# Performance work log

Measured on AMD Instinct MI355X. Metric: run time of the kernel, lower is better.

## Reference

```python
import jax, jax.numpy as jnp
import numpy as np

B, S, D = 4, 2048, 1024

def setup_inputs() -> dict:
    key = jax.random.key(0)
    ks = jax.random.split(key, 7)
    s = 1.0 / np.sqrt(D)
    return {
        "x":  jax.random.normal(ks[0], (B, S, D), dtype=jnp.float32),
        "Wq": jax.random.uniform(ks[1], (D, D), jnp.float32, -s, s),
        "bq": jax.random.uniform(ks[2], (D,),  jnp.float32, -s, s),
        "Wk": jax.random.uniform(ks[3], (D, D), jnp.float32, -s, s),
        "bk": jax.random.uniform(ks[4], (D,),  jnp.float32, -s, s),
        "Wv": jax.random.uniform(ks[5], (D, D), jnp.float32, -s, s),
        "bv": jax.random.uniform(ks[6], (D,),  jnp.float32, -s, s),
    }

def reference(x, Wq, bq, Wk, bk, Wv, bv):
    # Q/K/V projections: [B,S,D]
    Q = jnp.einsum('bsd,de->bse', x, Wq) + bq
    K = jnp.einsum('bsd,de->bse', x, Wk) + bk
    V = jnp.einsum('bsd,de->bse', x, Wv) + bv
    scale = 1.0 / jnp.sqrt(jnp.asarray(K.shape[-1], K.dtype))
    scores = jnp.einsum('bqd,bkd->bqk', Q, K) * scale  # [B,S,S]
    weights = jax.nn.softmax(scores, axis=-1)
    return jnp.einsum('bqk,bkd->bqd', weights, V)
```

## Files before the change

kernel.cpp:

```cpp
#include <hip/hip_runtime.h>

typedef __attribute__((ext_vector_type(4))) float f32x4;
typedef __attribute__((ext_vector_type(8))) short bf16x8;

__device__ __forceinline__ float bf2f(unsigned short u) {
  union { unsigned int i; float f; } x; x.i = ((unsigned int)u) << 16; return x.f;
}
__device__ __forceinline__ unsigned short f2bf(float f) {
  union { float f; unsigned int i; } x; x.f = f;
  unsigned int r = (x.i + 0x7FFFu + ((x.i >> 16) & 1u)) >> 16;
  return (unsigned short)r;
}

#define BARX __builtin_amdgcn_s_barrier()
#define LGK0 asm volatile("s_waitcnt lgkmcnt(0)" ::: "memory")
#define VM0  asm volatile("s_waitcnt vmcnt(0)" ::: "memory")
#define GLD(gsrc, ldsoff)                                                        \
  __builtin_amdgcn_global_load_lds(                                              \
      (const __attribute__((address_space(1))) void*)(gsrc),                     \
      (__attribute__((address_space(3))) void*)&lds[ldsoff], 16, 0, 0)

__global__ __launch_bounds__(256) void cvt_f2b(const float* __restrict__ src,
                                               unsigned short* __restrict__ dst, long n4) {
  long i = (long)blockIdx.x * 256 + threadIdx.x;
  long stride = (long)gridDim.x * 256;
  for (; i < n4; i += stride) {
    float4 v = *(const float4*)&src[i * 4];
    ushort4 o;
    o.x = f2bf(v.x); o.y = f2bf(v.y); o.z = f2bf(v.z); o.w = f2bf(v.w);
    *(ushort4*)&dst[i * 4] = o;
  }
}

__global__ __launch_bounds__(256) void transpose_f2b(const float* __restrict__ src,
                                                     unsigned short* __restrict__ dst,
                                                     int rows, int cols) {
  __shared__ float t[32][33];
  int bx = blockIdx.x * 32, by = blockIdx.y * 32;
  int tx = threadIdx.x, ty = threadIdx.y;
#pragma unroll
  for (int k = 0; k < 4; ++k)
    t[ty + 8 * k][tx] = src[(long)(by + ty + 8 * k) * cols + bx + tx];
  __syncthreads();
#pragma unroll
  for (int k = 0; k < 4; ++k)
    dst[(long)(bx + ty + 8 * k) * rows + by + tx] = f2bf(t[tx][ty + 8 * k]);
}

__global__ __launch_bounds__(512) void transpose_v(const unsigned short* __restrict__ src,
                                                   unsigned short* __restrict__ dst) {
  __shared__ unsigned short t[64][65];
  const long sb = (long)blockIdx.z * 2048 * 3072;
  const long db = (long)blockIdx.z * 1024 * 2064;
  const int d0 = blockIdx.x * 64;
  const int s0 = blockIdx.y * 64;
  const int tx = threadIdx.x, ty = threadIdx.y;
#pragma unroll
  for (int k = 0; k < 8; ++k)
    t[ty + 8 * k][tx] = src[sb + (long)(s0 + ty + 8 * k) * 3072 + d0 + tx];
  __syncthreads();
#pragma unroll
  for (int k = 0; k < 8; ++k)
    dst[db + (long)(d0 + ty + 8 * k) * 2064 + s0 + tx] = t[tx][ty + 8 * k];
}

template <int MODE>
__global__ __launch_bounds__(256, 2) void gemms(const unsigned short* __restrict__ Ap_,
                                                const unsigned short* __restrict__ Bp_,
                                                void* __restrict__ Cv,
                                                const float* __restrict__ q_,
                                                const float* __restrict__ k_,
                                                const float* __restrict__ v_,
                                                int Kd, int lda, int ldb, int ldc, float scale,
                                                long sA, long sB, long sC) {
  __shared__ unsigned short lds[32768];
  int bx, by, bz;
  if (MODE == 2) {
    const int flat = blockIdx.x;
    const int nid = ((flat & 7) << 6) | (flat >> 3);
    bx = nid & 15; by = (nid >> 4) & 7; bz = nid >> 7;
  } else {
    bx = blockIdx.x; by = blockIdx.y; bz = blockIdx.z;
  }
  const unsigned short* Ap = Ap_ + (long)bz * sA;
  const unsigned short* Bp = Bp_ + (long)bz * sB;
  const int tid = threadIdx.x;
  const int m0 = bx * 128, n0 = by * 128;
  const int lane = tid & 63, wave = tid >> 6;
  const int wm = wave >> 1, wn = wave & 1;
  const int rr = tid >> 3;
  const int cSrc = ((tid & 7) ^ (rr & 7)) << 3;
  const int lc = lane & 15, lr = lane >> 4;
  const int x0 = (lc & 4) << 3;
  const int x1 = 32 ^ x0;
  const int klo = (lr << 3) ^ ((lc & 3) << 3);
  const int aoff = (wm * 64 + lc) * 64 + klo;
  const int boff = 8192 + (wn * 64 + lc) * 64 + klo;
  const int NT = Kd >> 6;
  const int rS = tid >> 1;
  const int g0 = (tid & 1) * 4;

  const unsigned short* pA = Ap + (long)(m0 + rr) * lda + cSrc;
  const unsigned short* pB = Bp + (long)(n0 + rr) * ldb + cSrc;
  const long a32 = (long)32 * lda, b32 = (long)32 * ldb;
#define STA(so)                                                                   \
  { GLD(pA, (so) + tid * 8);            GLD(pA + a32, (so) + 2048 + tid * 8);     \
    GLD(pA + 2 * a32, (so) + 4096 + tid * 8); GLD(pA + 3 * a32, (so) + 6144 + tid * 8); }
#define STB(so)                                                                   \
  { GLD(pB, (so) + 8192 + tid * 8);     GLD(pB + b32, (so) + 10240 + tid * 8);    \
    GLD(pB + 2 * b32, (so) + 12288 + tid * 8); GLD(pB + 3 * b32, (so) + 14336 + tid * 8); }

  f32x4 acc[4][4] = {};
  float esum = 0.0f;

  STA(0); STB(0);
  pA += 64; pB += 64;
  VM0;
  BARX;

  for (int t = 0; t < NT; ++t) {
    const int p = t & 1;
    const int soq = (p ^ 1) << 14;
    const unsigned short* Lp = &lds[p << 14];
    const bool pf = (t + 1 < NT);
    bf16x8 a0[2][2], a1[2][2], bb[4][2];
#pragma unroll
    for (int ni = 0; ni < 4; ++ni) {
      bb[ni][0] = *(const bf16x8*)&Lp[boff + ni * 1024 + x0];
      bb[ni][1] = *(const bf16x8*)&Lp[boff + ni * 1024 + x1];
    }
#pragma unroll
    for (int mi = 0; mi < 2; ++mi) {
      a0[mi][0] = *(const bf16x8*)&Lp[aoff + mi * 1024 + x0];
      a0[mi][1] = *(const bf16x8*)&Lp[aoff + mi * 1024 + x1];
    }
    if (pf) STA(soq);
    BARX; LGK0;
    __builtin_amdgcn_s_setprio(1);
#pragma unroll
    for (int mi = 0; mi < 2; ++mi)
#pragma unroll
      for (int ni = 0; ni < 4; ++ni)
#pragma unroll
        for (int x = 0; x < 2; ++x)
          acc[mi][ni] = __builtin_amdgcn_mfma_f32_16x16x32_bf16(
              a0[mi][x], bb[ni][x], acc[mi][ni], 0, 0, 0);
    __builtin_amdgcn_s_setprio(0);
    BARX;
#pragma unroll
    for (int mi = 0; mi < 2; ++mi) {
      a1[mi][0] = *(const bf16x8*)&Lp[aoff + 2048 + mi * 1024 + x0];
      a1[mi][1] = *(const bf16x8*)&Lp[aoff + 2048 + mi * 1024 + x1];
    }
    if (MODE == 2) {
#pragma unroll
      for (int j = 0; j < 4; ++j) {
        bf16x8 s = *(const bf16x8*)&Lp[rS * 64 + (((g0 + j) ^ (rS & 7)) << 3)];
#pragma unroll
        for (int e = 0; e < 8; ++e) esum += bf2f((unsigned short)s[e]);
      }
    }
    if (pf) STB(soq);
    BARX; LGK0;
    __builtin_amdgcn_s_setprio(1);
#pragma unroll
    for (int mi = 0; mi < 2; ++mi)
#pragma unroll
      for (int ni = 0; ni < 4; ++ni)
#pragma unroll
        for (int x = 0; x < 2; ++x)
          acc[2 + mi][ni] = __builtin_amdgcn_mfma_f32_16x16x32_bf16(
              a1[mi][x], bb[ni][x], acc[2 + mi][ni], 0, 0, 0);
    __builtin_amdgcn_s_setprio(0);
    VM0;
    BARX;
    pA += 64; pB += 64;
  }
#undef STA
#undef STB

  const int r0 = m0 + wm * 64 + lr * 4;
  const int c0 = n0 + wn * 64 + lc;
  if (MODE == 2) {
    esum += __shfl_xor(esum, 1);
    float* sums = (float*)lds;
    if ((tid & 1) == 0) sums[tid >> 1] = esum;
    __syncthreads();
    float* O = (float*)Cv + (long)bz * sC;
#pragma unroll
    for (int mi = 0; mi < 4; ++mi)
#pragma unroll
      for (int r = 0; r < 4; ++r) {
        const int l = wm * 64 + mi * 16 + lr * 4 + r;
        const float iv = 1.0f / sums[l];
#pragma unroll
        for (int ni = 0; ni < 4; ++ni)
          O[(long)(m0 + l) * ldc + (c0 + ni * 16)] = acc[mi][ni][r] * iv;
      }
  } else {
    unsigned short* C = (unsigned short*)Cv + (long)bz * sC;
#pragma unroll
    for (int ni = 0; ni < 4; ++ni) {
      const int col = c0 + ni * 16;
      float bv = 0.0f;
      if (MODE == 0)
        bv = (col < 1024) ? q_[col] : ((col < 2048) ? k_[col - 1024] : v_[col - 2048]);
#pragma unroll
      for (int mi = 0; mi < 4; ++mi)
#pragma unroll
        for (int r = 0; r < 4; ++r) {
          float val = acc[mi][ni][r];
          val = (MODE == 0) ? (val + bv) : __expf(val * scale);
          C[(long)(r0 + mi * 16 + r) * ldc + col] = f2bf(val);
        }
    }
  }
}

extern "C" void kernel_launch(void* const* d_in, const int* in_sizes, int n_in,
                              void* d_out, int out_size, void* d_ws, size_t ws_size,
                              hipStream_t stream) {
  const float* x  = (const float*)d_in[0];
  const float* Wq = (const float*)d_in[1];
  const float* bq = (const float*)d_in[2];
  const float* Wk = (const float*)d_in[3];
  const float* bk = (const float*)d_in[4];
  const float* Wv = (const float*)d_in[5];
  const float* bv = (const float*)d_in[6];
  float* out = (float*)d_out;

  const int Bb = 4, S = 2048, D = 1024;
  const long MS = (long)Bb * S;
  const int LDP = 2064;

  char* ws = (char*)d_ws;
  unsigned short* xb  = (unsigned short*)(ws);
  unsigned short* Wt  = (unsigned short*)(ws + (16L << 20));
  unsigned short* QKV = (unsigned short*)(ws + (22L << 20));
  unsigned short* Sc  = (unsigned short*)(ws + (70L << 20));
  unsigned short* VT  = xb;

  cvt_f2b<<<2048, 256, 0, stream>>>(x, xb, MS * D / 4);

  dim3 tb(32, 8);
  dim3 tg(D / 32, D / 32);
  transpose_f2b<<<tg, tb, 0, stream>>>(Wq, Wt, D, D);
  transpose_f2b<<<tg, tb, 0, stream>>>(Wk, Wt + 1024 * 1024, D, D);
  transpose_f2b<<<tg, tb, 0, stream>>>(Wv, Wt + 2 * 1024 * 1024, D, D);

  dim3 pgrid(MS / 128, 3072 / 128, 1);
  gemms<0><<<pgrid, 256, 0, stream>>>(xb, Wt, QKV, bq, bk, bv,
                                      D, D, D, 3072, 1.0f, 0, 0, 0);

  dim3 vtb(64, 8);
  dim3 vtg(D / 64, S / 64, Bb);
  transpose_v<<<vtg, vtb, 0, stream>>>(QKV + 2048, VT);

  dim3 sgrid(S / 128, S / 128, Bb);
  gemms<1><<<sgrid, 256, 0, stream>>>(QKV, QKV + 1024, Sc, nullptr, nullptr, nullptr,
                                      D, 3072, 3072, LDP, 1.0f / 32.0f,
                                      (long)S * 3072, (long)S * 3072, (long)S * LDP);

  gemms<2><<<512, 256, 0, stream>>>(Sc, VT, out, nullptr, nullptr, nullptr,
                                    2048, LDP, LDP, D, 1.0f,
                                    (long)S * LDP, (long)D * LDP, (long)S * D);
}
```

Before: 173.2 us.

## Restructure GEMM main loop into 4-stage BK=32 pipeline with MFMA row sums

After: 195.0 us. 12.6% more time.

```diff
diff --git a/kernel.cpp b/kernel.cpp
--- a/kernel.cpp
+++ b/kernel.cpp
@@ -14,7 +14,6 @@
 
 #define BARX __builtin_amdgcn_s_barrier()
 #define LGK0 asm volatile("s_waitcnt lgkmcnt(0)" ::: "memory")
-#define VM0  asm volatile("s_waitcnt vmcnt(0)" ::: "memory")
 #define GLD(gsrc, ldsoff)                                                        \
   __builtin_amdgcn_global_load_lds(                                              \
       (const __attribute__((address_space(1))) void*)(gsrc),                     \
@@ -65,7 +64,7 @@
 }
 
 template <int MODE>
-__global__ __launch_bounds__(256, 2) void gemms(const unsigned short* __restrict__ Ap_,
+__global__ __launch_bounds__(256, 2) void gemmk(const unsigned short* __restrict__ Ap_,
                                                 const unsigned short* __restrict__ Bp_,
                                                 void* __restrict__ Cv,
                                                 const float* __restrict__ q_,
@@ -82,120 +81,80 @@
   } else {
     bx = blockIdx.x; by = blockIdx.y; bz = blockIdx.z;
   }
-  const unsigned short* Ap = Ap_ + (long)bz * sA;
-  const unsigned short* Bp = Bp_ + (long)bz * sB;
   const int tid = threadIdx.x;
   const int m0 = bx * 128, n0 = by * 128;
   const int lane = tid & 63, wave = tid >> 6;
   const int wm = wave >> 1, wn = wave & 1;
-  const int rr = tid >> 3;
-  const int cSrc = ((tid & 7) ^ (rr & 7)) << 3;
+  const int rrS = tid >> 2;
+  const int gS = (((tid & 3) ^ ((tid >> 2) & 3)) << 3);
   const int lc = lane & 15, lr = lane >> 4;
-  const int x0 = (lc & 4) << 3;
-  const int x1 = 32 ^ x0;
-  const int klo = (lr << 3) ^ ((lc & 3) << 3);
-  const int aoff = (wm * 64 + lc) * 64 + klo;
-  const int boff = 8192 + (wn * 64 + lc) * 64 + klo;
-  const int NT = Kd >> 6;
-  const int rS = tid >> 1;
-  const int g0 = (tid & 1) * 4;
-
-  const unsigned short* pA = Ap + (long)(m0 + rr) * lda + cSrc;
-  const unsigned short* pB = Bp + (long)(n0 + rr) * ldb + cSrc;
-  const long a32 = (long)32 * lda, b32 = (long)32 * ldb;
-#define STA(so)                                                                   \
-  { GLD(pA, (so) + tid * 8);            GLD(pA + a32, (so) + 2048 + tid * 8);     \
-    GLD(pA + 2 * a32, (so) + 4096 + tid * 8); GLD(pA + 3 * a32, (so) + 6144 + tid * 8); }
-#define STB(so)                                                                   \
-  { GLD(pB, (so) + 8192 + tid * 8);     GLD(pB + b32, (so) + 10240 + tid * 8);    \
-    GLD(pB + 2 * b32, (so) + 12288 + tid * 8); GLD(pB + 3 * b32, (so) + 14336 + tid * 8); }
+  const int kof = ((lr ^ (lc & 3)) << 3);
+  const int aoff = (wm * 64 + lc) * 32 + kof;
+  const int boff = 4096 + (wn * 64 + lc) * 32 + kof;
+  const int NT = Kd >> 5;
+
+  const unsigned short* pA0 = Ap_ + (long)bz * sA + (long)(m0 + rrS) * lda + gS;
+  const unsigned short* pA1 = pA0 + (long)64 * lda;
+  const unsigned short* pB0 = Bp_ + (long)bz * sB + (long)(n0 + rrS) * ldb + gS;
+  const unsigned short* pB1 = pB0 + (long)64 * ldb;
+#define STAGE(so)                                                                 \
+  { GLD(pA0, (so) + tid * 8);        GLD(pA1, (so) + 2048 + tid * 8);             \
+    GLD(pB0, (so) + 4096 + tid * 8); GLD(pB1, (so) + 6144 + tid * 8); }
+#define ADV { pA0 += 32; pA1 += 32; pB0 += 32; pB1 += 32; }
 
   f32x4 acc[4][4] = {};
-  float esum = 0.0f;
-
-  STA(0); STB(0);
-  pA += 64; pB += 64;
-  VM0;
+  f32x4 es[4] = {};
+  bf16x8 ones;
+#pragma unroll
+  for (int j = 0; j < 8; ++j) ones[j] = (short)0x3F80;
+
+  STAGE(0); ADV;
+  STAGE(8192); ADV;
+  asm volatile("s_waitcnt vmcnt(4)" ::: "memory");
   BARX;
 
   for (int t = 0; t < NT; ++t) {
-    const int p = t & 1;
-    const int soq = (p ^ 1) << 14;
-    const unsigned short* Lp = &lds[p << 14];
-    const bool pf = (t + 1 < NT);
-    bf16x8 a0[2][2], a1[2][2], bb[4][2];
-#pragma unroll
-    for (int ni = 0; ni < 4; ++ni) {
-      bb[ni][0] = *(const bf16x8*)&Lp[boff + ni * 1024 + x0];
-      bb[ni][1] = *(const bf16x8*)&Lp[boff + ni * 1024 + x1];
+    const int Lb = (t & 3) << 13;
+    const bool pf = (t + 2 < NT);
+    bf16x8 a[4], b[4];
+#pragma unroll
+    for (int mi = 0; mi < 4; ++mi) a[mi] = *(const bf16x8*)&lds[Lb + aoff + mi * 512];
+#pragma unroll
+    for (int ni = 0; ni < 4; ++ni) b[ni] = *(const bf16x8*)&lds[Lb + boff + ni * 512];
+    if (pf) { const int so = ((t + 2) & 3) << 13; STAGE(so); }
+    LGK0;
+    __builtin_amdgcn_s_setprio(1);
+#pragma unroll
+    for (int mi = 0; mi < 4; ++mi)
+#pragma unroll
+      for (int ni = 0; ni < 4; ++ni)
+        acc[mi][ni] = __builtin_amdgcn_mfma_f32_16x16x32_bf16(a[mi], b[ni], acc[mi][ni], 0, 0, 0);
+    if (MODE == 2) {
+#pragma unroll
+      for (int mi = 0; mi < 4; ++mi)
+        es[mi] = __builtin_amdgcn_mfma_f32_16x16x32_bf16(a[mi], ones, es[mi], 0, 0, 0);
     }
-#pragma unroll
-    for (int mi = 0; mi < 2; ++mi) {
-      a0[mi][0] = *(const bf16x8*)&Lp[aoff + mi * 1024 + x0];
-      a0[mi][1] = *(const bf16x8*)&Lp[aoff + mi * 1024 + x1];
-    }
-    if (pf) STA(soq);
-    BARX; LGK0;
-    __builtin_amdgcn_s_setprio(1);
-#pragma unroll
-    for (int mi = 0; mi < 2; ++mi)
-#pragma unroll
-      for (int ni = 0; ni < 4; ++ni)
-#pragma unroll
-        for (int x = 0; x < 2; ++x)
-          acc[mi][ni] = __builtin_amdgcn_mfma_f32_16x16x32_bf16(
-              a0[mi][x], bb[ni][x], acc[mi][ni], 0, 0, 0);
     __builtin_amdgcn_s_setprio(0);
+    if (pf) { asm volatile("s_waitcnt vmcnt(4)" ::: "memory"); }
+    else    { asm volatile("s_waitcnt vmcnt(0)" ::: "memory"); }
     BARX;
-#pragma unroll
-    for (int mi = 0; mi < 2; ++mi) {
-      a1[mi][0] = *(const bf16x8*)&Lp[aoff + 2048 + mi * 1024 + x0];
-      a1[mi][1] = *(const bf16x8*)&Lp[aoff + 2048 + mi * 1024 + x1];
-    }
-    if (MODE == 2) {
-#pragma unroll
-      for (int j = 0; j < 4; ++j) {
-        bf16x8 s = *(const bf16x8*)&Lp[rS * 64 + (((g0 + j) ^ (rS & 7)) << 3)];
-#pragma unroll
-        for (int e = 0; e < 8; ++e) esum += bf2f((unsigned short)s[e]);
-      }
-    }
-    if (pf) STB(soq);
-    BARX; LGK0;
-    __builtin_amdgcn_s_setprio(1);
-#pragma unroll
-    for (int mi = 0; mi < 2; ++mi)
-#pragma unroll
-      for (int ni = 0; ni < 4; ++ni)
-#pragma unroll
-        for (int x = 0; x < 2; ++x)
-          acc[2 + mi][ni] = __builtin_amdgcn_mfma_f32_16x16x32_bf16(
-              a1[mi][x], bb[ni][x], acc[2 + mi][ni], 0, 0, 0);
-    __builtin_amdgcn_s_setprio(0);
-    VM0;
-    BARX;
-    pA += 64; pB += 64;
-  }
-#undef STA
-#undef STB
+    ADV;
+  }
+#undef STAGE
+#undef ADV
 
   const int r0 = m0 + wm * 64 + lr * 4;
   const int c0 = n0 + wn * 64 + lc;
   if (MODE == 2) {
-    esum += __shfl_xor(esum, 1);
-    float* sums = (float*)lds;
-    if ((tid & 1) == 0) sums[tid >> 1] = esum;
-    __syncthreads();
     float* O = (float*)Cv + (long)bz * sC;
 #pragma unroll
     for (int mi = 0; mi < 4; ++mi)
 #pragma unroll
       for (int r = 0; r < 4; ++r) {
-        const int l = wm * 64 + mi * 16 + lr * 4 + r;
-        const float iv = 1.0f / sums[l];
+        const float iv = 1.0f / es[mi][r];
 #pragma unroll
         for (int ni = 0; ni < 4; ++ni)
-          O[(long)(m0 + l) * ldc + (c0 + ni * 16)] = acc[mi][ni][r] * iv;
+          O[(long)(r0 + mi * 16 + r) * ldc + (c0 + ni * 16)] = acc[mi][ni][r] * iv;
       }
   } else {
     unsigned short* C = (unsigned short*)Cv + (long)bz * sC;
@@ -249,7 +208,7 @@
   transpose_f2b<<<tg, tb, 0, stream>>>(Wv, Wt + 2 * 1024 * 1024, D, D);
 
   dim3 pgrid(MS / 128, 3072 / 128, 1);
-  gemms<0><<<pgrid, 256, 0, stream>>>(xb, Wt, QKV, bq, bk, bv,
+  gemmk<0><<<pgrid, 256, 0, stream>>>(xb, Wt, QKV, bq, bk, bv,
                                       D, D, D, 3072, 1.0f, 0, 0, 0);
 
   dim3 vtb(64, 8);
@@ -257,11 +216,11 @@
   transpose_v<<<vtg, vtb, 0, stream>>>(QKV + 2048, VT);
 
   dim3 sgrid(S / 128, S / 128, Bb);
-  gemms<1><<<sgrid, 256, 0, stream>>>(QKV, QKV + 1024, Sc, nullptr, nullptr, nullptr,
+  gemmk<1><<<sgrid, 256, 0, stream>>>(QKV, QKV + 1024, Sc, nullptr, nullptr, nullptr,
                                       D, 3072, 3072, LDP, 1.0f / 32.0f,
                                       (long)S * 3072, (long)S * 3072, (long)S * LDP);
 
-  gemms<2><<<512, 256, 0, stream>>>(Sc, VT, out, nullptr, nullptr, nullptr,
+  gemmk<2><<<512, 256, 0, stream>>>(Sc, VT, out, nullptr, nullptr, nullptr,
                                     2048, LDP, LDP, D, 1.0f,
                                     (long)S * LDP, (long)D * LDP, (long)S * D);
 }
```

## Single-buffer GEMM LDS for higher occupancy and compute row sums via MFMA

Applied to the files above, without the earlier changes.

After: 423.9 us. 145% more time.

```diff
diff --git a/kernel.cpp b/kernel.cpp
--- a/kernel.cpp
+++ b/kernel.cpp
@@ -13,7 +13,6 @@
 }
 
 #define BARX __builtin_amdgcn_s_barrier()
-#define LGK0 asm volatile("s_waitcnt lgkmcnt(0)" ::: "memory")
 #define VM0  asm volatile("s_waitcnt vmcnt(0)" ::: "memory")
 #define GLD(gsrc, ldsoff)                                                        \
   __builtin_amdgcn_global_load_lds(                                              \
@@ -65,7 +64,7 @@
 }
 
 template <int MODE>
-__global__ __launch_bounds__(256, 2) void gemms(const unsigned short* __restrict__ Ap_,
+__global__ __launch_bounds__(256, 4) void gemmo(const unsigned short* __restrict__ Ap_,
                                                 const unsigned short* __restrict__ Bp_,
                                                 void* __restrict__ Cv,
                                                 const float* __restrict__ q_,
@@ -73,7 +72,7 @@
                                                 const float* __restrict__ v_,
                                                 int Kd, int lda, int ldb, int ldc, float scale,
                                                 long sA, long sB, long sC) {
-  __shared__ unsigned short lds[32768];
+  __shared__ unsigned short lds[16384];
   int bx, by, bz;
   if (MODE == 2) {
     const int flat = blockIdx.x;
@@ -82,8 +81,6 @@
   } else {
     bx = blockIdx.x; by = blockIdx.y; bz = blockIdx.z;
   }
-  const unsigned short* Ap = Ap_ + (long)bz * sA;
-  const unsigned short* Bp = Bp_ + (long)bz * sB;
   const int tid = threadIdx.x;
   const int m0 = bx * 128, n0 = by * 128;
   const int lane = tid & 63, wave = tid >> 6;
@@ -97,45 +94,35 @@
   const int aoff = (wm * 64 + lc) * 64 + klo;
   const int boff = 8192 + (wn * 64 + lc) * 64 + klo;
   const int NT = Kd >> 6;
-  const int rS = tid >> 1;
-  const int g0 = (tid & 1) * 4;
-
-  const unsigned short* pA = Ap + (long)(m0 + rr) * lda + cSrc;
-  const unsigned short* pB = Bp + (long)(n0 + rr) * ldb + cSrc;
+
+  const unsigned short* pA = Ap_ + (long)bz * sA + (long)(m0 + rr) * lda + cSrc;
+  const unsigned short* pB = Bp_ + (long)bz * sB + (long)(n0 + rr) * ldb + cSrc;
   const long a32 = (long)32 * lda, b32 = (long)32 * ldb;
-#define STA(so)                                                                   \
-  { GLD(pA, (so) + tid * 8);            GLD(pA + a32, (so) + 2048 + tid * 8);     \
-    GLD(pA + 2 * a32, (so) + 4096 + tid * 8); GLD(pA + 3 * a32, (so) + 6144 + tid * 8); }
-#define STB(so)                                                                   \
-  { GLD(pB, (so) + 8192 + tid * 8);     GLD(pB + b32, (so) + 10240 + tid * 8);    \
-    GLD(pB + 2 * b32, (so) + 12288 + tid * 8); GLD(pB + 3 * b32, (so) + 14336 + tid * 8); }
 
   f32x4 acc[4][4] = {};
-  float esum = 0.0f;
-
-  STA(0); STB(0);
-  pA += 64; pB += 64;
-  VM0;
-  BARX;
+  f32x4 es[4] = {};
+  bf16x8 ones;
+#pragma unroll
+  for (int j = 0; j < 8; ++j) ones[j] = (short)0x3F80;
 
   for (int t = 0; t < NT; ++t) {
-    const int p = t & 1;
-    const int soq = (p ^ 1) << 14;
-    const unsigned short* Lp = &lds[p << 14];
-    const bool pf = (t + 1 < NT);
+    GLD(pA, tid * 8);            GLD(pA + a32, 2048 + tid * 8);
+    GLD(pA + 2 * a32, 4096 + tid * 8); GLD(pA + 3 * a32, 6144 + tid * 8);
+    GLD(pB, 8192 + tid * 8);     GLD(pB + b32, 10240 + tid * 8);
+    GLD(pB + 2 * b32, 12288 + tid * 8); GLD(pB + 3 * b32, 14336 + tid * 8);
+    VM0;
+    BARX;
     bf16x8 a0[2][2], a1[2][2], bb[4][2];
 #pragma unroll
     for (int ni = 0; ni < 4; ++ni) {
-      bb[ni][0] = *(const bf16x8*)&Lp[boff + ni * 1024 + x0];
-      bb[ni][1] = *(const bf16x8*)&Lp[boff + ni * 1024 + x1];
+      bb[ni][0] = *(const bf16x8*)&lds[boff + ni * 1024 + x0];
+      bb[ni][1] = *(const bf16x8*)&lds[boff + ni * 1024 + x1];
     }
 #pragma unroll
     for (int mi = 0; mi < 2; ++mi) {
-      a0[mi][0] = *(const bf16x8*)&Lp[aoff + mi * 1024 + x0];
-      a0[mi][1] = *(const bf16x8*)&Lp[aoff + mi * 1024 + x1];
-    }
-    if (pf) STA(soq);
-    BARX; LGK0;
+      a0[mi][0] = *(const bf16x8*)&lds[aoff + mi * 1024 + x0];
+      a0[mi][1] = *(const bf16x8*)&lds[aoff + mi * 1024 + x1];
+    }
     __builtin_amdgcn_s_setprio(1);
 #pragma unroll
     for (int mi = 0; mi < 2; ++mi)
@@ -145,57 +132,52 @@
         for (int x = 0; x < 2; ++x)
           acc[mi][ni] = __builtin_amdgcn_mfma_f32_16x16x32_bf16(
               a0[mi][x], bb[ni][x], acc[mi][ni], 0, 0, 0);
+    if (MODE == 2) {
+#pragma unroll
+      for (int mi = 0; mi < 2; ++mi)
+#pragma unroll
+        for (int x = 0; x < 2; ++x)
+          es[mi] = __builtin_amdgcn_mfma_f32_16x16x32_bf16(a0[mi][x], ones, es[mi], 0, 0, 0);
+    }
+    __builtin_amdgcn_s_setprio(0);
+#pragma unroll
+    for (int mi = 0; mi < 2; ++mi) {
+      a1[mi][0] = *(const bf16x8*)&lds[aoff + 2048 + mi * 1024 + x0];
+      a1[mi][1] = *(const bf16x8*)&lds[aoff + 2048 + mi * 1024 + x1];
+    }
+    __builtin_amdgcn_s_setprio(1);
+#pragma unroll
+    for (int mi = 0; mi < 2; ++mi)
+#pragma unroll
+      for (int ni = 0; ni < 4; ++ni)
+#pragma unroll
+        for (int x = 0; x < 2; ++x)
+          acc[2 + mi][ni] = __builtin_amdgcn_mfma_f32_16x16x32_bf16(
+              a1[mi][x], bb[ni][x], acc[2 + mi][ni], 0, 0, 0);
+    if (MODE == 2) {
+#pragma unroll
+      for (int mi = 0; mi < 2; ++mi)
+#pragma unroll
+        for (int x = 0; x < 2; ++x)
+          es[2 + mi] = __builtin_amdgcn_mfma_f32_16x16x32_bf16(a1[mi][x], ones, es[2 + mi], 0, 0, 0);
+    }
     __builtin_amdgcn_s_setprio(0);
     BARX;
-#pragma unroll
-    for (int mi = 0; mi < 2; ++mi) {
-      a1[mi][0] = *(const bf16x8*)&Lp[aoff + 2048 + mi * 1024 + x0];
-      a1[mi][1] = *(const bf16x8*)&Lp[aoff + 2048 + mi * 1024 + x1];
-    }
-    if (MODE == 2) {
-#pragma unroll
-      for (int j = 0; j < 4; ++j) {
-        bf16x8 s = *(const bf16x8*)&Lp[rS * 64 + (((g0 + j) ^ (rS & 7)) << 3)];
-#pragma unroll
-        for (int e = 0; e < 8; ++e) esum += bf2f((unsigned short)s[e]);
-      }
-    }
-    if (pf) STB(soq);
-    BARX; LGK0;
-    __builtin_amdgcn_s_setprio(1);
-#pragma unroll
-    for (int mi = 0; mi < 2; ++mi)
-#pragma unroll
-      for (int ni = 0; ni < 4; ++ni)
-#pragma unroll
-        for (int x = 0; x < 2; ++x)
-          acc[2 + mi][ni] = __builtin_amdgcn_mfma_f32_16x16x32_bf16(
-              a1[mi][x], bb[ni][x], acc[2 + mi][ni], 0, 0, 0);
-    __builtin_amdgcn_s_setprio(0);
-    VM0;
-    BARX;
     pA += 64; pB += 64;
   }
-#undef STA
-#undef STB
 
   const int r0 = m0 + wm * 64 + lr * 4;
   const int c0 = n0 + wn * 64 + lc;
   if (MODE == 2) {
-    esum += __shfl_xor(esum, 1);
-    float* sums = (float*)lds;
-    if ((tid & 1) == 0) sums[tid >> 1] = esum;
-    __syncthreads();
     float* O = (float*)Cv + (long)bz * sC;
 #pragma unroll
     for (int mi = 0; mi < 4; ++mi)
 #pragma unroll
       for (int r = 0; r < 4; ++r) {
-        const int l = wm * 64 + mi * 16 + lr * 4 + r;
-        const float iv = 1.0f / sums[l];
+        const float iv = 1.0f / es[mi][r];
 #pragma unroll
         for (int ni = 0; ni < 4; ++ni)
-          O[(long)(m0 + l) * ldc + (c0 + ni * 16)] = acc[mi][ni][r] * iv;
+          O[(long)(r0 + mi * 16 + r) * ldc + (c0 + ni * 16)] = acc[mi][ni][r] * iv;
       }
   } else {
     unsigned short* C = (unsigned short*)Cv + (long)bz * sC;
@@ -249,7 +231,7 @@
   transpose_f2b<<<tg, tb, 0, stream>>>(Wv, Wt + 2 * 1024 * 1024, D, D);
 
   dim3 pgrid(MS / 128, 3072 / 128, 1);
-  gemms<0><<<pgrid, 256, 0, stream>>>(xb, Wt, QKV, bq, bk, bv,
+  gemmo<0><<<pgrid, 256, 0, stream>>>(xb, Wt, QKV, bq, bk, bv,
                                       D, D, D, 3072, 1.0f, 0, 0, 0);
 
   dim3 vtb(64, 8);
@@ -257,11 +239,11 @@
   transpose_v<<<vtg, vtb, 0, stream>>>(QKV + 2048, VT);
 
   dim3 sgrid(S / 128, S / 128, Bb);
-  gemms<1><<<sgrid, 256, 0, stream>>>(QKV, QKV + 1024, Sc, nullptr, nullptr, nullptr,
+  gemmo<1><<<sgrid, 256, 0, stream>>>(QKV, QKV + 1024, Sc, nullptr, nullptr, nullptr,
                                       D, 3072, 3072, LDP, 1.0f / 32.0f,
                                       (long)S * 3072, (long)S * 3072, (long)S * LDP);
 
-  gemms<2><<<512, 256, 0, stream>>>(Sc, VT, out, nullptr, nullptr, nullptr,
+  gemmo<2><<<512, 256, 0, stream>>>(Sc, VT, out, nullptr, nullptr, nullptr,
                                     2048, LDP, LDP, D, 1.0f,
                                     (long)S * LDP, (long)D * LDP, (long)S * D);
 }
```
